# Performance work log

Hardware: AMD Instinct MI355X
Metric: run time of the kernel (lower is better)

Reference implementation:

```python
import jax, jax.numpy as jnp
import numpy as np

IN_CH = 256
BOT = IN_CH // 2  # bottleneck channels
B, W, H = 4, 64, 64


def setup_inputs() -> dict:
    key = jax.random.key(0)
    ks = jax.random.split(key, 10)
    s_in = 1.0 / np.sqrt(IN_CH)   # torch Conv2d default init scale (kaiming-ish bound)
    s_bt = 1.0 / np.sqrt(BOT)
    return {
        "X": jax.random.normal(ks[0], (B, IN_CH, W, H), dtype=jnp.float32),
        "Wq": jax.random.uniform(ks[1], (BOT, IN_CH), jnp.float32, -s_in, s_in),
        "bq": jax.random.uniform(ks[2], (BOT,), jnp.float32, -s_in, s_in),
        "Wk": jax.random.uniform(ks[3], (BOT, IN_CH), jnp.float32, -s_in, s_in),
        "bk": jax.random.uniform(ks[4], (BOT,), jnp.float32, -s_in, s_in),
        "Wv": jax.random.uniform(ks[5], (BOT, IN_CH), jnp.float32, -s_in, s_in),
        "bv": jax.random.uniform(ks[6], (BOT,), jnp.float32, -s_in, s_in),
        "Wo": jax.random.uniform(ks[7], (IN_CH, BOT), jnp.float32, -s_bt, s_bt),
        "bo": jax.random.uniform(ks[8], (IN_CH,), jnp.float32, -s_bt, s_bt),
        "gamma": 0.1 * jax.random.normal(ks[9], (1,), dtype=jnp.float32),
    }


def reference(X, Wq, bq, Wk, bk, Wv, bv, Wo, bo, gamma):
    b, c, w, h = X.shape
    n = w * h
    Xf = X.reshape(b, c, n)  # [b, c, n] — 1x1 conv == per-pixel linear
    q = jnp.einsum('oc,bcn->bon', Wq, Xf) + bq[None, :, None]  # [b, c/2, n]
    k = jnp.einsum('oc,bcn->bon', Wk, Xf) + bk[None, :, None]
    v = jnp.einsum('oc,bcn->bon', Wv, Xf) + bv[None, :, None]
    # score[b,i,j] = sum_c q[b,c,i] * k[b,c,j]; softmax over dim=1 (query index i)
    score = jnp.einsum('bci,bcj->bij', q, k)          # [b, n, n]
    attn = jax.nn.softmax(score, axis=1)
    out = jnp.einsum('bci,bij->bcj', v, attn)         # [b, c/2, n]
    out = jnp.einsum('oc,bcn->bon', Wo, out) + bo[None, :, None]  # [b, c, n]
    out = out.reshape(b, c, w, h)
    return gamma[0] * out + X
```

## Files before the change

kernel.cpp:

```cpp
#include <hip/hip_runtime.h>
#include <math.h>

#define NBATCH 4
#define CIN    256
#define CBOT   128
#define NPIX   4096
#define NPART  6
#define LOG2E  1.44269504f

typedef __attribute__((ext_vector_type(4))) float f32x4;
typedef __attribute__((ext_vector_type(8))) short bf16x8;

__device__ __forceinline__ unsigned short f2bf(float f) {
    union { float f; unsigned u; } v; v.f = f;
    unsigned r = (v.u + 0x7FFFu + ((v.u >> 16) & 1u)) >> 16;
    return (unsigned short)r;
}
__device__ __forceinline__ unsigned pk2bf(float a, float b) {
#if __has_builtin(__builtin_amdgcn_cvt_pk_bf16_f32)
    auto r = __builtin_amdgcn_cvt_pk_bf16_f32(a, b);
    unsigned u; __builtin_memcpy(&u, &r, 4); return u;
#else
    unsigned r;
    asm("v_cvt_pk_bf16_f32 %0, %1, %2" : "=v"(r) : "v"(a), "v"(b));
    return r;
#endif
}
__device__ __forceinline__ float fexp2(float x) {
#if __has_builtin(__builtin_amdgcn_exp2f)
    return __builtin_amdgcn_exp2f(x);
#else
    float r;
    asm("v_exp_f32 %0, %1" : "=v"(r) : "v"(x));
    return r;
#endif
}
__device__ __forceinline__ void plswap32(unsigned &a, unsigned &b) {
#if __has_builtin(__builtin_amdgcn_permlane32_swap)
    auto r = __builtin_amdgcn_permlane32_swap(a, b, false, false);
    a = (unsigned)r[0]; b = (unsigned)r[1];
#else
    asm volatile("v_permlane32_swap_b32 %0, %1" : "+v"(a), "+v"(b));
#endif
}
__device__ __forceinline__ void plswap16(unsigned &a, unsigned &b) {
#if __has_builtin(__builtin_amdgcn_permlane16_swap)
    auto r = __builtin_amdgcn_permlane16_swap(a, b, false, false);
    a = (unsigned)r[0]; b = (unsigned)r[1];
#else
    asm volatile("v_permlane16_swap_b32 %0, %1" : "+v"(a), "+v"(b));
#endif
}

__global__ __launch_bounds__(256) void k_wcvt(
    const float* __restrict__ Wq, const float* __restrict__ Wk,
    const float* __restrict__ Wv, const float* __restrict__ Wo,
    unsigned short* __restrict__ Wb)
{
    const int f4 = (blockIdx.x * 256 + threadIdx.x) * 4;
    const int reg = f4 >> 15, loc = f4 & 32767;
    const float* __restrict__ W = (reg == 0) ? Wq : (reg == 1) ? Wk : (reg == 2) ? Wv : Wo;
    const float sc = (reg == 1) ? LOG2E : 1.f;
    float4 v = *(const float4*)(W + loc);
    uint2 u;
    u.x = pk2bf(v.x * sc, v.y * sc);
    u.y = pk2bf(v.z * sc, v.w * sc);
    *(uint2*)&Wb[f4] = u;
}

__global__ __launch_bounds__(256) void k_qkvx(
    const float* __restrict__ X,
    const unsigned short* __restrict__ Wb,
    const float* __restrict__ bq, const float* __restrict__ bk,
    const float* __restrict__ bv,
    unsigned short* __restrict__ Qt, unsigned short* __restrict__ Kt,
    unsigned short* __restrict__ Vt)
{
    __shared__ __align__(16) unsigned short Xs[32][264];
    const int tid = threadIdx.x;
    const int wv = tid >> 6, lane = tid & 63;
    const int grp = lane & 15, quad = lane >> 4;
    const int pbase = blockIdx.x * 32;
    const int b     = blockIdx.y;
    const float* __restrict__ Xg = X + (size_t)b * CIN * NPIX + pbase;

#pragma unroll
    for (int k = 0; k < 8; ++k) {
        int f = tid + 256 * k;
        int c = f >> 3, pg = (f & 7) << 2;
        float4 v = *(const float4*)(Xg + (size_t)c * NPIX + pg);
        unsigned uxy = pk2bf(v.x, v.y);
        unsigned uzw = pk2bf(v.z, v.w);
        Xs[pg + 0][c] = (unsigned short)uxy;
        Xs[pg + 1][c] = (unsigned short)(uxy >> 16);
        Xs[pg + 2][c] = (unsigned short)uzw;
        Xs[pg + 3][c] = (unsigned short)(uzw >> 16);
    }
    __syncthreads();

    const unsigned short* __restrict__ Wqb = Wb;
    const unsigned short* __restrict__ Wkb = Wb + 32768;
    const unsigned short* __restrict__ Wvb = Wb + 65536;
    const int obase = 32 * wv;

    f32x4 aQ[2][2], aK[2][2], aV[2][2];
#pragma unroll
    for (int mt = 0; mt < 2; ++mt)
#pragma unroll
        for (int nt = 0; nt < 2; ++nt) {
            aQ[mt][nt] = (f32x4)0.f; aK[mt][nt] = (f32x4)0.f; aV[mt][nt] = (f32x4)0.f;
        }

    for (int ks = 0; ks < 8; ++ks) {
        bf16x8 bx[2];
#pragma unroll
        for (int nt = 0; nt < 2; ++nt)
            bx[nt] = *(const bf16x8*)&Xs[nt * 16 + grp][ks * 32 + quad * 8];
        bf16x8 wq_[2], wk_[2], wv_[2];
#pragma unroll
        for (int mt = 0; mt < 2; ++mt) {
            const size_t roff = (size_t)(obase + mt * 16 + grp) * CIN + ks * 32 + quad * 8;
            wq_[mt] = *(const bf16x8*)&Wqb[roff];
            wk_[mt] = *(const bf16x8*)&Wkb[roff];
            wv_[mt] = *(const bf16x8*)&Wvb[roff];
        }
#pragma unroll
        for (int mt = 0; mt < 2; ++mt)
#pragma unroll
            for (int nt = 0; nt < 2; ++nt) {
                aQ[mt][nt] = __builtin_amdgcn_mfma_f32_16x16x32_bf16(wq_[mt], bx[nt], aQ[mt][nt], 0, 0, 0);
                aK[mt][nt] = __builtin_amdgcn_mfma_f32_16x16x32_bf16(wk_[mt], bx[nt], aK[mt][nt], 0, 0, 0);
                aV[mt][nt] = __builtin_amdgcn_mfma_f32_16x16x32_bf16(bx[mt], wv_[nt], aV[mt][nt], 0, 0, 0);
            }
    }

    unsigned short* Qb_ = Qt + (size_t)b * NPIX * CBOT;
    unsigned short* Kb_ = Kt + (size_t)b * NPIX * CBOT;
#pragma unroll
    for (int mt = 0; mt < 2; ++mt) {
        int o0 = obase + mt * 16 + quad * 4;
        float b4q[4], b4k[4];
#pragma unroll
        for (int r = 0; r < 4; ++r) { b4q[r] = bq[o0 + r]; b4k[r] = bk[o0 + r] * LOG2E; }
#pragma unroll
        for (int nt = 0; nt < 2; ++nt) {
            int p = pbase + nt * 16 + grp;
            uint2 uq, uk;
            uq.x = pk2bf(aQ[mt][nt][0] + b4q[0], aQ[mt][nt][1] + b4q[1]);
            uq.y = pk2bf(aQ[mt][nt][2] + b4q[2], aQ[mt][nt][3] + b4q[3]);
            uk.x = pk2bf(aK[mt][nt][0] + b4k[0], aK[mt][nt][1] + b4k[1]);
            uk.y = pk2bf(aK[mt][nt][2] + b4k[2], aK[mt][nt][3] + b4k[3]);
            *(uint2*)&Qb_[(size_t)p * CBOT + o0] = uq;
            *(uint2*)&Kb_[(size_t)p * CBOT + o0] = uk;
        }
    }
    unsigned short* Vb_ = Vt + (size_t)b * CBOT * NPIX;
#pragma unroll
    for (int nt = 0; nt < 2; ++nt) {
        int o = obase + nt * 16 + grp;
        float bb = bv[o];
#pragma unroll
        for (int mt = 0; mt < 2; ++mt) {
            int p0 = pbase + mt * 16 + quad * 4;
            uint2 u;
            u.x = pk2bf(aV[mt][nt][0] + bb, aV[mt][nt][1] + bb);
            u.y = pk2bf(aV[mt][nt][2] + bb, aV[mt][nt][3] + bb);
            *(uint2*)&Vb_[(size_t)o * NPIX + p0] = u;
        }
    }
}

__global__ __launch_bounds__(256, 3) void k_flash(
    const unsigned short* __restrict__ Qt,
    const unsigned short* __restrict__ Kt,
    const unsigned short* __restrict__ Vt,
    unsigned short* __restrict__ Opart,
    float* __restrict__ Lpart)
{
    __shared__ __align__(16) unsigned short Qs[64][136];
    __shared__ __align__(16) unsigned short Vs[128][72];
    const int tid  = threadIdx.x;
    const int wv   = tid >> 6, lane = tid & 63;
    const int grp  = lane & 15, quad = lane >> 4;

    const int x    = blockIdx.x;
    const int y    = blockIdx.y;
    const int z    = blockIdx.z;
    const int g    = x & 7;
    const int u    = y * 16 + ((x >> 3) + 4 * z);
    const int pair = g * 3 + (u >> 5);
    const int jp   = u & 31;
    const int b    = pair / 6;
    const int part = pair % 6;
    const int jblk = jp * 128;
    const int tbeg = (part * 32) / 3;
    const int tend = ((part + 1) * 32) / 3;
    const unsigned short* __restrict__ Qb = Qt + (size_t)b * NPIX * CBOT;
    const unsigned short* __restrict__ Kb = Kt + (size_t)b * NPIX * CBOT;
    const unsigned short* __restrict__ Vb = Vt + (size_t)b * CBOT * NPIX;

    bf16x8 bk[2][4];
#pragma unroll
    for (int nt = 0; nt < 2; ++nt)
#pragma unroll
        for (int ks = 0; ks < 4; ++ks)
            bk[nt][ks] = *(const bf16x8*)&Kb[
                (size_t)(jblk + wv * 32 + nt * 16 + grp) * CBOT + ks * 32 + quad * 8];

    bf16x8 aones;
#pragma unroll
    for (int t = 0; t < 8; ++t) aones[t] = (short)0x3F80;

    f32x4 o[8][2];
#pragma unroll
    for (int ct = 0; ct < 8; ++ct) { o[ct][0] = (f32x4)0.f; o[ct][1] = (f32x4)0.f; }
    f32x4 lacc[2] = {(f32x4)0.f, (f32x4)0.f};

    const int qrow = tid >> 4, qch = tid & 15;
    const int vrow = tid >> 3, vch = tid & 7;

    {
        bf16x8 tq[4], tv[4];
#pragma unroll
        for (int k = 0; k < 4; ++k) {
            tq[k] = *(const bf16x8*)&Qb[(size_t)(tbeg * 64 + qrow + 16 * k) * CBOT + qch * 8];
            tv[k] = *(const bf16x8*)&Vb[(size_t)(vrow + 32 * k) * NPIX + tbeg * 64 + vch * 8];
        }
#pragma unroll
        for (int k = 0; k < 4; ++k) {
            *(bf16x8*)&Qs[qrow + 16 * k][qch * 8] = tq[k];
            *(bf16x8*)&Vs[vrow + 32 * k][vch * 8] = tv[k];
        }
    }
    __syncthreads();

    for (int it = tbeg; it < tend; ++it) {
        f32x4 sf[4][2];
#pragma unroll
        for (int mt = 0; mt < 4; ++mt) { sf[mt][0] = (f32x4)0.f; sf[mt][1] = (f32x4)0.f; }
        __builtin_amdgcn_s_setprio(1);
#pragma unroll
        for (int mt = 0; mt < 4; ++mt)
#pragma unroll
            for (int ks = 0; ks < 4; ++ks) {
                bf16x8 aq_ = *(const bf16x8*)&Qs[mt * 16 + grp][ks * 32 + quad * 8];
                sf[mt][0] = __builtin_amdgcn_mfma_f32_16x16x32_bf16(aq_, bk[0][ks], sf[mt][0], 0, 0, 0);
                sf[mt][1] = __builtin_amdgcn_mfma_f32_16x16x32_bf16(aq_, bk[1][ks], sf[mt][1], 0, 0, 0);
            }
        __builtin_amdgcn_s_setprio(0);

        bf16x8 pf[2][2];
#pragma unroll
        for (int nt = 0; nt < 2; ++nt)
#pragma unroll
            for (int h = 0; h < 2; ++h) {
                unsigned u0a = pk2bf(fexp2(sf[2 * h][nt][0]),     fexp2(sf[2 * h][nt][1]));
                unsigned u1a = pk2bf(fexp2(sf[2 * h][nt][2]),     fexp2(sf[2 * h][nt][3]));
                unsigned u0b = pk2bf(fexp2(sf[2 * h + 1][nt][0]), fexp2(sf[2 * h + 1][nt][1]));
                unsigned u1b = pk2bf(fexp2(sf[2 * h + 1][nt][2]), fexp2(sf[2 * h + 1][nt][3]));
                plswap32(u0a, u0b); plswap16(u0a, u0b);
                plswap32(u1a, u1b); plswap16(u1a, u1b);
                union { unsigned uu[4]; bf16x8 v; } cvt;
                cvt.uu[0] = u0a; cvt.uu[1] = u1a; cvt.uu[2] = u0b; cvt.uu[3] = u1b;
                pf[nt][h] = cvt.v;
            }

        __builtin_amdgcn_s_setprio(1);
#pragma unroll
        for (int ct = 0; ct < 8; ++ct)
#pragma unroll
            for (int h = 0; h < 2; ++h) {
                bf16x8 av_ = *(const bf16x8*)&Vs[ct * 16 + grp][h * 32 + quad * 8];
                o[ct][0] = __builtin_amdgcn_mfma_f32_16x16x32_bf16(av_, pf[0][h], o[ct][0], 0, 0, 0);
                o[ct][1] = __builtin_amdgcn_mfma_f32_16x16x32_bf16(av_, pf[1][h], o[ct][1], 0, 0, 0);
            }
#pragma unroll
        for (int nt = 0; nt < 2; ++nt) {
            lacc[nt] = __builtin_amdgcn_mfma_f32_16x16x32_bf16(aones, pf[nt][0], lacc[nt], 0, 0, 0);
            lacc[nt] = __builtin_amdgcn_mfma_f32_16x16x32_bf16(aones, pf[nt][1], lacc[nt], 0, 0, 0);
        }
        __builtin_amdgcn_s_setprio(0);

        if (it + 1 < tend) {
            bf16x8 tq[4], tv[4];
            const size_t i1 = (size_t)(it + 1) * 64;
#pragma unroll
            for (int k = 0; k < 4; ++k) {
                tq[k] = *(const bf16x8*)&Qb[(i1 + qrow + 16 * k) * CBOT + qch * 8];
                tv[k] = *(const bf16x8*)&Vb[(size_t)(vrow + 32 * k) * NPIX + i1 + vch * 8];
            }
            __syncthreads();
#pragma unroll
            for (int k = 0; k < 4; ++k) {
                *(bf16x8*)&Qs[qrow + 16 * k][qch * 8] = tq[k];
                *(bf16x8*)&Vs[vrow + 32 * k][vch * 8] = tv[k];
            }
            __syncthreads();
        }
    }

    const int pbI = part * NBATCH + b;
    unsigned short* Ob = Opart + ((size_t)pbI * NPIX + jblk) * CBOT;
#pragma unroll
    for (int nt = 0; nt < 2; ++nt) {
        const size_t jrow = (size_t)(wv * 32 + nt * 16 + grp) * CBOT;
#pragma unroll
        for (int ct = 0; ct < 8; ++ct) {
            uint2 uo;
            uo.x = pk2bf(o[ct][nt][0], o[ct][nt][1]);
            uo.y = pk2bf(o[ct][nt][2], o[ct][nt][3]);
            *(uint2*)&Ob[jrow + ct * 16 + quad * 4] = uo;
        }
    }
    if (quad == 0) {
#pragma unroll
        for (int nt = 0; nt < 2; ++nt)
            Lpart[(size_t)pbI * NPIX + jblk + wv * 32 + nt * 16 + grp] =
                lacc[nt][0];
    }
}

__global__ __launch_bounds__(256) void k_oproj(
    const unsigned short* __restrict__ Opart, const float* __restrict__ Lpart,
    const unsigned short* __restrict__ Wob, const float* __restrict__ bo,
    const float* __restrict__ gamma, const float* __restrict__ X,
    float* __restrict__ Out)
{
    const int tid = threadIdx.x;
    const int wv = tid >> 6, lane = tid & 63;
    const int grp = lane & 15, quad = lane >> 4;
    const int pbase = blockIdx.x * 32;
    const int b     = blockIdx.y;
    const int obase = 64 * wv;

    f32x4 acc[2][4];
#pragma unroll
    for (int mt = 0; mt < 2; ++mt)
#pragma unroll
        for (int nt = 0; nt < 4; ++nt) acc[mt][nt] = (f32x4)0.f;

    for (int ks = 0; ks < 4; ++ks) {
        bf16x8 bw[4];
#pragma unroll
        for (int nt = 0; nt < 4; ++nt)
            bw[nt] = *(const bf16x8*)&Wob[(size_t)(obase + nt * 16 + grp) * CBOT + ks * 32 + quad * 8];
#pragma unroll
        for (int mt = 0; mt < 2; ++mt) {
            int p = pbase + mt * 16 + grp;
#pragma unroll
            for (int part = 0; part < NPART; ++part) {
                bf16x8 ao = *(const bf16x8*)&Opart[
                    ((size_t)(part * NBATCH + b) * NPIX + p) * CBOT + ks * 32 + quad * 8];
#pragma unroll
                for (int nt = 0; nt < 4; ++nt)
                    acc[mt][nt] = __builtin_amdgcn_mfma_f32_16x16x32_bf16(ao, bw[nt], acc[mt][nt], 0, 0, 0);
            }
        }
    }

    float linv[2][4];
#pragma unroll
    for (int mt = 0; mt < 2; ++mt)
#pragma unroll
        for (int r = 0; r < 4; ++r) {
            int p = pbase + mt * 16 + quad * 4 + r;
            float ls = 0.f;
#pragma unroll
            for (int part = 0; part < NPART; ++part)
                ls += Lpart[(size_t)(part * NBATCH + b) * NPIX + p];
            linv[mt][r] = 1.f / ls;
        }
    float gm = gamma[0];
#pragma unroll
    for (int nt = 0; nt < 4; ++nt) {
        int o = obase + nt * 16 + grp;
        float bb = bo[o];
#pragma unroll
        for (int mt = 0; mt < 2; ++mt) {
            int p0 = pbase + mt * 16 + quad * 4;
            size_t base = (size_t)b * CIN * NPIX + (size_t)o * NPIX + p0;
            float4 x4 = *(const float4*)(X + base);
            float4 r4;
            r4.x = gm * (acc[mt][nt][0] * linv[mt][0] + bb) + x4.x;
            r4.y = gm * (acc[mt][nt][1] * linv[mt][1] + bb) + x4.y;
            r4.z = gm * (acc[mt][nt][2] * linv[mt][2] + bb) + x4.z;
            r4.w = gm * (acc[mt][nt][3] * linv[mt][3] + bb) + x4.w;
            *(float4*)(Out + base) = r4;
        }
    }
}

extern "C" void kernel_launch(void* const* d_in, const int* in_sizes, int n_in,
                              void* d_out, int out_size, void* d_ws, size_t ws_size,
                              hipStream_t stream)
{
    (void)in_sizes; (void)n_in; (void)out_size; (void)ws_size;
    const float* X     = (const float*)d_in[0];
    const float* Wq    = (const float*)d_in[1];
    const float* bq    = (const float*)d_in[2];
    const float* Wk    = (const float*)d_in[3];
    const float* bk    = (const float*)d_in[4];
    const float* Wv    = (const float*)d_in[5];
    const float* bv    = (const float*)d_in[6];
    const float* Wo    = (const float*)d_in[7];
    const float* bo    = (const float*)d_in[8];
    const float* gamma = (const float*)d_in[9];
    float* out = (float*)d_out;

    const size_t BNC = (size_t)NBATCH * NPIX * CBOT;
    unsigned short* Qt    = (unsigned short*)d_ws;
    unsigned short* Kt    = Qt + BNC;
    unsigned short* Vt    = Kt + BNC;
    unsigned short* Opart = Vt + BNC;
    float*          Lpart = (float*)(Opart + (size_t)NPART * BNC);
    unsigned short* Wb    = (unsigned short*)(Lpart + (size_t)NPART * NBATCH * NPIX);

    k_wcvt <<<dim3(128),               256, 0, stream>>>(Wq, Wk, Wv, Wo, Wb);
    k_qkvx <<<dim3(128, NBATCH),       256, 0, stream>>>(X, Wb, bq, bk, bv, Qt, Kt, Vt);
    k_flash<<<dim3(32, NPART, NBATCH), 256, 0, stream>>>(Qt, Kt, Vt, Opart, Lpart);
    k_oproj<<<dim3(128, NBATCH),       256, 0, stream>>>(Opart, Lpart, Wb + 98304, bo, gamma, X, out);
}
```

Baseline: 159.8 us.

## Prefetch next Q/V tiles into registers in flash loop and shrink projection tiles

In the flash kernel, the Q and V tiles for the iteration after next are loaded from global memory into registers right after the current shared-memory store, so the global load latency overlaps the MFMA work. Launch bounds drop from 3 to 2 blocks per SM to leave room for the extra live registers. The QKV and output projection kernels now use 16-pixel tiles instead of 32 and launch twice as many blocks, for more parallelism at the cost of less weight reuse per block.

```diff
diff --git a/kernel.cpp b/kernel.cpp
--- a/kernel.cpp
+++ b/kernel.cpp
@@ -76,18 +76,18 @@
     unsigned short* __restrict__ Qt, unsigned short* __restrict__ Kt,
     unsigned short* __restrict__ Vt)
 {
-    __shared__ __align__(16) unsigned short Xs[32][264];
+    __shared__ __align__(16) unsigned short Xs[16][264];
     const int tid = threadIdx.x;
     const int wv = tid >> 6, lane = tid & 63;
     const int grp = lane & 15, quad = lane >> 4;
-    const int pbase = blockIdx.x * 32;
+    const int pbase = blockIdx.x * 16;
     const int b     = blockIdx.y;
     const float* __restrict__ Xg = X + (size_t)b * CIN * NPIX + pbase;
 
 #pragma unroll
-    for (int k = 0; k < 8; ++k) {
+    for (int k = 0; k < 4; ++k) {
         int f = tid + 256 * k;
-        int c = f >> 3, pg = (f & 7) << 2;
+        int c = f >> 2, pg = (f & 3) << 2;
         float4 v = *(const float4*)(Xg + (size_t)c * NPIX + pg);
         unsigned uxy = pk2bf(v.x, v.y);
         unsigned uzw = pk2bf(v.z, v.w);
@@ -103,19 +103,12 @@
     const unsigned short* __restrict__ Wvb = Wb + 65536;
     const int obase = 32 * wv;
 
-    f32x4 aQ[2][2], aK[2][2], aV[2][2];
-#pragma unroll
-    for (int mt = 0; mt < 2; ++mt)
-#pragma unroll
-        for (int nt = 0; nt < 2; ++nt) {
-            aQ[mt][nt] = (f32x4)0.f; aK[mt][nt] = (f32x4)0.f; aV[mt][nt] = (f32x4)0.f;
-        }
+    f32x4 aQ[2], aK[2], aV[2];
+#pragma unroll
+    for (int mt = 0; mt < 2; ++mt) { aQ[mt] = (f32x4)0.f; aK[mt] = (f32x4)0.f; aV[mt] = (f32x4)0.f; }
 
     for (int ks = 0; ks < 8; ++ks) {
-        bf16x8 bx[2];
-#pragma unroll
-        for (int nt = 0; nt < 2; ++nt)
-            bx[nt] = *(const bf16x8*)&Xs[nt * 16 + grp][ks * 32 + quad * 8];
+        bf16x8 bx = *(const bf16x8*)&Xs[grp][ks * 32 + quad * 8];
         bf16x8 wq_[2], wk_[2], wv_[2];
 #pragma unroll
         for (int mt = 0; mt < 2; ++mt) {
@@ -125,13 +118,11 @@
             wv_[mt] = *(const bf16x8*)&Wvb[roff];
         }
 #pragma unroll
-        for (int mt = 0; mt < 2; ++mt)
-#pragma unroll
-            for (int nt = 0; nt < 2; ++nt) {
-                aQ[mt][nt] = __builtin_amdgcn_mfma_f32_16x16x32_bf16(wq_[mt], bx[nt], aQ[mt][nt], 0, 0, 0);
-                aK[mt][nt] = __builtin_amdgcn_mfma_f32_16x16x32_bf16(wk_[mt], bx[nt], aK[mt][nt], 0, 0, 0);
-                aV[mt][nt] = __builtin_amdgcn_mfma_f32_16x16x32_bf16(bx[mt], wv_[nt], aV[mt][nt], 0, 0, 0);
-            }
+        for (int mt = 0; mt < 2; ++mt) {
+            aQ[mt] = __builtin_amdgcn_mfma_f32_16x16x32_bf16(wq_[mt], bx, aQ[mt], 0, 0, 0);
+            aK[mt] = __builtin_amdgcn_mfma_f32_16x16x32_bf16(wk_[mt], bx, aK[mt], 0, 0, 0);
+            aV[mt] = __builtin_amdgcn_mfma_f32_16x16x32_bf16(bx, wv_[mt], aV[mt], 0, 0, 0);
+        }
     }
 
     unsigned short* Qb_ = Qt + (size_t)b * NPIX * CBOT;
@@ -142,35 +133,29 @@
         float b4q[4], b4k[4];
 #pragma unroll
         for (int r = 0; r < 4; ++r) { b4q[r] = bq[o0 + r]; b4k[r] = bk[o0 + r] * LOG2E; }
-#pragma unroll
-        for (int nt = 0; nt < 2; ++nt) {
-            int p = pbase + nt * 16 + grp;
-            uint2 uq, uk;
-            uq.x = pk2bf(aQ[mt][nt][0] + b4q[0], aQ[mt][nt][1] + b4q[1]);
-            uq.y = pk2bf(aQ[mt][nt][2] + b4q[2], aQ[mt][nt][3] + b4q[3]);
-            uk.x = pk2bf(aK[mt][nt][0] + b4k[0], aK[mt][nt][1] + b4k[1]);
-            uk.y = pk2bf(aK[mt][nt][2] + b4k[2], aK[mt][nt][3] + b4k[3]);
-            *(uint2*)&Qb_[(size_t)p * CBOT + o0] = uq;
-            *(uint2*)&Kb_[(size_t)p * CBOT + o0] = uk;
-        }
+        int p = pbase + grp;
+        uint2 uq, uk;
+        uq.x = pk2bf(aQ[mt][0] + b4q[0], aQ[mt][1] + b4q[1]);
+        uq.y = pk2bf(aQ[mt][2] + b4q[2], aQ[mt][3] + b4q[3]);
+        uk.x = pk2bf(aK[mt][0] + b4k[0], aK[mt][1] + b4k[1]);
+        uk.y = pk2bf(aK[mt][2] + b4k[2], aK[mt][3] + b4k[3]);
+        *(uint2*)&Qb_[(size_t)p * CBOT + o0] = uq;
+        *(uint2*)&Kb_[(size_t)p * CBOT + o0] = uk;
     }
     unsigned short* Vb_ = Vt + (size_t)b * CBOT * NPIX;
 #pragma unroll
     for (int nt = 0; nt < 2; ++nt) {
         int o = obase + nt * 16 + grp;
         float bb = bv[o];
-#pragma unroll
-        for (int mt = 0; mt < 2; ++mt) {
-            int p0 = pbase + mt * 16 + quad * 4;
-            uint2 u;
-            u.x = pk2bf(aV[mt][nt][0] + bb, aV[mt][nt][1] + bb);
-            u.y = pk2bf(aV[mt][nt][2] + bb, aV[mt][nt][3] + bb);
-            *(uint2*)&Vb_[(size_t)o * NPIX + p0] = u;
-        }
-    }
-}
-
-__global__ __launch_bounds__(256, 3) void k_flash(
+        int p0 = pbase + quad * 4;
+        uint2 u;
+        u.x = pk2bf(aV[nt][0] + bb, aV[nt][1] + bb);
+        u.y = pk2bf(aV[nt][2] + bb, aV[nt][3] + bb);
+        *(uint2*)&Vb_[(size_t)o * NPIX + p0] = u;
+    }
+}
+
+__global__ __launch_bounds__(256, 2) void k_flash(
     const unsigned short* __restrict__ Qt,
     const unsigned short* __restrict__ Kt,
     const unsigned short* __restrict__ Vt,
@@ -218,18 +203,23 @@
 
     const int qrow = tid >> 4, qch = tid & 15;
     const int vrow = tid >> 3, vch = tid & 7;
-
+    bf16x8 qreg[4], vreg[4];
+#pragma unroll
+    for (int k = 0; k < 4; ++k) {
+        qreg[k] = *(const bf16x8*)&Qb[(size_t)(tbeg * 64 + qrow + 16 * k) * CBOT + qch * 8];
+        vreg[k] = *(const bf16x8*)&Vb[(size_t)(vrow + 32 * k) * NPIX + tbeg * 64 + vch * 8];
+    }
+#pragma unroll
+    for (int k = 0; k < 4; ++k) {
+        *(bf16x8*)&Qs[qrow + 16 * k][qch * 8] = qreg[k];
+        *(bf16x8*)&Vs[vrow + 32 * k][vch * 8] = vreg[k];
+    }
     {
-        bf16x8 tq[4], tv[4];
+        const int i1 = (tbeg + 1) * 64;
 #pragma unroll
         for (int k = 0; k < 4; ++k) {
-            tq[k] = *(const bf16x8*)&Qb[(size_t)(tbeg * 64 + qrow + 16 * k) * CBOT + qch * 8];
-            tv[k] = *(const bf16x8*)&Vb[(size_t)(vrow + 32 * k) * NPIX + tbeg * 64 + vch * 8];
-        }
-#pragma unroll
-        for (int k = 0; k < 4; ++k) {
-            *(bf16x8*)&Qs[qrow + 16 * k][qch * 8] = tq[k];
-            *(bf16x8*)&Vs[vrow + 32 * k][vch * 8] = tv[k];
+            qreg[k] = *(const bf16x8*)&Qb[(size_t)(i1 + qrow + 16 * k) * CBOT + qch * 8];
+            vreg[k] = *(const bf16x8*)&Vb[(size_t)(vrow + 32 * k) * NPIX + i1 + vch * 8];
         }
     }
     __syncthreads();
@@ -282,18 +272,19 @@
         __builtin_amdgcn_s_setprio(0);
 
         if (it + 1 < tend) {
-            bf16x8 tq[4], tv[4];
-            const size_t i1 = (size_t)(it + 1) * 64;
+            __syncthreads();
 #pragma unroll
             for (int k = 0; k < 4; ++k) {
-                tq[k] = *(const bf16x8*)&Qb[(i1 + qrow + 16 * k) * CBOT + qch * 8];
-                tv[k] = *(const bf16x8*)&Vb[(size_t)(vrow + 32 * k) * NPIX + i1 + vch * 8];
+                *(bf16x8*)&Qs[qrow + 16 * k][qch * 8] = qreg[k];
+                *(bf16x8*)&Vs[vrow + 32 * k][vch * 8] = vreg[k];
             }
-            __syncthreads();
-#pragma unroll
-            for (int k = 0; k < 4; ++k) {
-                *(bf16x8*)&Qs[qrow + 16 * k][qch * 8] = tq[k];
-                *(bf16x8*)&Vs[vrow + 32 * k][vch * 8] = tv[k];
+            if (it + 2 < tend) {
+                const int i2 = (it + 2) * 64;
+#pragma unroll
+                for (int k = 0; k < 4; ++k) {
+                    qreg[k] = *(const bf16x8*)&Qb[(size_t)(i2 + qrow + 16 * k) * CBOT + qch * 8];
+                    vreg[k] = *(const bf16x8*)&Vb[(size_t)(vrow + 32 * k) * NPIX + i2 + vch * 8];
+                }
             }
             __syncthreads();
         }
@@ -329,64 +320,54 @@
     const int tid = threadIdx.x;
     const int wv = tid >> 6, lane = tid & 63;
     const int grp = lane & 15, quad = lane >> 4;
-    const int pbase = blockIdx.x * 32;
+    const int pbase = blockIdx.x * 16;
     const int b     = blockIdx.y;
     const int obase = 64 * wv;
 
-    f32x4 acc[2][4];
-#pragma unroll
-    for (int mt = 0; mt < 2; ++mt)
-#pragma unroll
-        for (int nt = 0; nt < 4; ++nt) acc[mt][nt] = (f32x4)0.f;
+    f32x4 acc[4];
+#pragma unroll
+    for (int nt = 0; nt < 4; ++nt) acc[nt] = (f32x4)0.f;
 
     for (int ks = 0; ks < 4; ++ks) {
         bf16x8 bw[4];
 #pragma unroll
         for (int nt = 0; nt < 4; ++nt)
             bw[nt] = *(const bf16x8*)&Wob[(size_t)(obase + nt * 16 + grp) * CBOT + ks * 32 + quad * 8];
-#pragma unroll
-        for (int mt = 0; mt < 2; ++mt) {
-            int p = pbase + mt * 16 + grp;
-#pragma unroll
-            for (int part = 0; part < NPART; ++part) {
-                bf16x8 ao = *(const bf16x8*)&Opart[
-                    ((size_t)(part * NBATCH + b) * NPIX + p) * CBOT + ks * 32 + quad * 8];
-#pragma unroll
-                for (int nt = 0; nt < 4; ++nt)
-                    acc[mt][nt] = __builtin_amdgcn_mfma_f32_16x16x32_bf16(ao, bw[nt], acc[mt][nt], 0, 0, 0);
-            }
-        }
-    }
-
-    float linv[2][4];
-#pragma unroll
-    for (int mt = 0; mt < 2; ++mt)
-#pragma unroll
-        for (int r = 0; r < 4; ++r) {
-            int p = pbase + mt * 16 + quad * 4 + r;
-            float ls = 0.f;
-#pragma unroll
-            for (int part = 0; part < NPART; ++part)
-                ls += Lpart[(size_t)(part * NBATCH + b) * NPIX + p];
-            linv[mt][r] = 1.f / ls;
-        }
+        const int p = pbase + grp;
+#pragma unroll
+        for (int part = 0; part < NPART; ++part) {
+            bf16x8 ao = *(const bf16x8*)&Opart[
+                ((size_t)(part * NBATCH + b) * NPIX + p) * CBOT + ks * 32 + quad * 8];
+#pragma unroll
+            for (int nt = 0; nt < 4; ++nt)
+                acc[nt] = __builtin_amdgcn_mfma_f32_16x16x32_bf16(ao, bw[nt], acc[nt], 0, 0, 0);
+        }
+    }
+
+    float linv[4];
+#pragma unroll
+    for (int r = 0; r < 4; ++r) {
+        int p = pbase + quad * 4 + r;
+        float ls = 0.f;
+#pragma unroll
+        for (int part = 0; part < NPART; ++part)
+            ls += Lpart[(size_t)(part * NBATCH + b) * NPIX + p];
+        linv[r] = 1.f / ls;
+    }
     float gm = gamma[0];
 #pragma unroll
     for (int nt = 0; nt < 4; ++nt) {
         int o = obase + nt * 16 + grp;
         float bb = bo[o];
-#pragma unroll
-        for (int mt = 0; mt < 2; ++mt) {
-            int p0 = pbase + mt * 16 + quad * 4;
-            size_t base = (size_t)b * CIN * NPIX + (size_t)o * NPIX + p0;
-            float4 x4 = *(const float4*)(X + base);
-            float4 r4;
-            r4.x = gm * (acc[mt][nt][0] * linv[mt][0] + bb) + x4.x;
-            r4.y = gm * (acc[mt][nt][1] * linv[mt][1] + bb) + x4.y;
-            r4.z = gm * (acc[mt][nt][2] * linv[mt][2] + bb) + x4.z;
-            r4.w = gm * (acc[mt][nt][3] * linv[mt][3] + bb) + x4.w;
-            *(float4*)(Out + base) = r4;
-        }
+        int p0 = pbase + quad * 4;
+        size_t base = (size_t)b * CIN * NPIX + (size_t)o * NPIX + p0;
+        float4 x4 = *(const float4*)(X + base);
+        float4 r4;
+        r4.x = gm * (acc[nt][0] * linv[0] + bb) + x4.x;
+        r4.y = gm * (acc[nt][1] * linv[1] + bb) + x4.y;
+        r4.z = gm * (acc[nt][2] * linv[2] + bb) + x4.z;
+        r4.w = gm * (acc[nt][3] * linv[3] + bb) + x4.w;
+        *(float4*)(Out + base) = r4;
     }
 }
 
@@ -416,7 +397,7 @@
     unsigned short* Wb    = (unsigned short*)(Lpart + (size_t)NPART * NBATCH * NPIX);
 
     k_wcvt <<<dim3(128),               256, 0, stream>>>(Wq, Wk, Wv, Wo, Wb);
-    k_qkvx <<<dim3(128, NBATCH),       256, 0, stream>>>(X, Wb, bq, bk, bv, Qt, Kt, Vt);
+    k_qkvx <<<dim3(256, NBATCH),       256, 0, stream>>>(X, Wb, bq, bk, bv, Qt, Kt, Vt);
     k_flash<<<dim3(32, NPART, NBATCH), 256, 0, stream>>>(Qt, Kt, Vt, Opart, Lpart);
-    k_oproj<<<dim3(128, NBATCH),       256, 0, stream>>>(Opart, Lpart, Wb + 98304, bo, gamma, X, out);
-}
+    k_oproj<<<dim3(256, NBATCH),       256, 0, stream>>>(Opart, Lpart, Wb + 98304, bo, gamma, X, out);
+}
```

After: 181.8 us. 13.7% more time.
